# Optimization experiments

Hardware: AMD Instinct MI355X
Metric: run time of the kernel (lower is better)

The kernel has to match this reference:

```python
import jax, jax.numpy as jnp
import numpy as np

SCALES = (5, 15, 40)


def _hamilton(a, b):
    # a, b: (..., 4) quaternions in [w, x, y, z]
    aw, ax, ay, az = a[..., 0], a[..., 1], a[..., 2], a[..., 3]
    bw, bx, by, bz = b[..., 0], b[..., 1], b[..., 2], b[..., 3]
    return jnp.stack([
        aw * bw - ax * bx - ay * by - az * bz,
        aw * bx + ax * bw + ay * bz - az * by,
        aw * by - ax * bz + ay * bw + az * bx,
        aw * bz + ax * by - ay * bx + az * bw,
    ], axis=-1)


def _bearing_quaternions(xyz):
    # xyz: (B, F, P, 3) -> bearing quaternions (B, F, P, 4)
    bbox_min = xyz.min(axis=2)
    bbox_max = xyz.max(axis=2)
    centroids = (bbox_min + bbox_max) * 0.5  # (B, F, 3)
    d = xyz - centroids[:, :, None, :]
    d = d / jnp.clip(jnp.linalg.norm(d, axis=-1, keepdims=True), 1e-12)
    dot = jnp.clip(d[..., 1], -1.0 + 1e-7, 1.0 - 1e-7)
    half = jnp.arccos(dot) * 0.5
    axis = jnp.stack([d[..., 2], jnp.zeros_like(d[..., 0]), -d[..., 0]], axis=-1)
    axis = axis / jnp.clip(jnp.linalg.norm(axis, axis=-1, keepdims=True), 1e-12)
    s = jnp.sin(half)
    return jnp.stack([jnp.cos(half), axis[..., 0] * s, axis[..., 1] * s, axis[..., 2] * s], axis=-1)


def _torch_lower_median(x):
    flat = jnp.sort(x.reshape(-1))
    return flat[(flat.shape[0] - 1) // 2]


def _bearing_qcc_multiscale(points_4d, num_frames):
    B, F, P, _ = points_4d.shape
    xyz = points_4d[..., :3]  # (B, F, P, 3)
    bq = _bearing_quaternions(xyz)  # (B, F, P, 4)

    # Per-transition relative quaternion q_fwd = q_tgt * conj(q_src), vectorized over T = F-1
    conj_sign = jnp.array([1.0, -1.0, -1.0, -1.0], dtype=points_4d.dtype)
    q_src = bq[:, :-1] * conj_sign  # conj, (B, T, P, 4)
    q_tgt = bq[:, 1:]
    q_fwd = _hamilton(q_tgt, q_src)
    q_fwd = q_fwd / jnp.clip(jnp.linalg.norm(q_fwd, axis=-1, keepdims=True), 1e-12)

    # KNN on source-frame xyz for all transitions at once (topk is sorted desc,
    # so smaller-k neighborhoods are prefixes of the max-k result)
    pts = xyz[:, :-1]  # (B, T, P, 3)
    sq = jnp.sum(pts * pts, axis=-1)  # (B, T, P)
    neg_dist = 2.0 * jnp.einsum('btpc,btqc->btpq', pts, pts) - sq[..., :, None] - sq[..., None, :]
    kmax = max(SCALES)
    _, idx = jax.lax.top_k(neg_dist, kmax)  # (B, T, P, kmax)

    # Gather neighbor quaternions: (B, T, P, kmax, 4)
    b_ix = jnp.arange(B)[:, None, None, None]
    t_ix = jnp.arange(F - 1)[None, :, None, None]
    nbr_q = q_fwd[b_ix, t_ix, idx]

    dots = jnp.abs(jnp.sum(q_fwd[..., None, :] * nbr_q, axis=-1))
    dots = jnp.clip(dots, 0.0, 1.0 - 1e-7)
    geo = 2.0 * jnp.arccos(dots)  # (B, T, P, kmax)

    rigidities = []
    for k in SCALES:
        mean_inc = geo[..., :k].mean(axis=-1).mean(axis=1)  # (B, P)
        scale = jnp.clip(_torch_lower_median(mean_inc), 1e-6)
        rig = jnp.where(mean_inc.max() > 0,
                        jnp.exp(-mean_inc / scale),
                        jnp.ones_like(mean_inc))  # (B, P)
        rig = jnp.broadcast_to(rig[:, None, :], (B, F, P)).reshape(B, 1, F * P)
        rigidities.append(rig)
    return jnp.concatenate(rigidities, axis=1)  # (B, len(SCALES), F*P)


def setup_inputs() -> dict:
    key = jax.random.key(0)
    B, F, P = 2, 8, 2048
    points_4d = jax.random.normal(key, (B, F, P, 4), dtype=jnp.float32)
    return {"points_4d": points_4d, "num_frames": F}


def reference(points_4d, num_frames):
    return _bearing_qcc_multiscale(points_4d, num_frames)
```

## Files before the change

### kernel.cpp

```cpp
#include <hip/hip_runtime.h>
#include <math.h>

typedef unsigned long long u64;
typedef unsigned int u32;

#define B_ 2
#define F_ 8
#define P_ 2048
#define T_ 7
#define ROWS (B_*T_*P_)
#define SENT_OU 0xFFFFFFFFu

#define CED(arr,a,b) do { double _x=arr[a], _y=arr[b]; arr[a]=fmin(_x,_y); arr[b]=fmax(_x,_y); } while(0)

__device__ __forceinline__ void sort8d(double* k) {
  CED(k,0,1); CED(k,2,3); CED(k,4,5); CED(k,6,7);
  CED(k,0,2); CED(k,1,3); CED(k,4,6); CED(k,5,7);
  CED(k,1,2); CED(k,5,6);
  CED(k,0,4); CED(k,1,5); CED(k,2,6); CED(k,3,7);
  CED(k,2,4); CED(k,3,5);
  CED(k,1,2); CED(k,3,4); CED(k,5,6);
}

__device__ __forceinline__ void low8(double* A, const double* Bv) {
#pragma unroll
  for (int i = 0; i < 8; ++i) A[i] = fmin(A[i], Bv[7-i]);
#pragma unroll
  for (int st = 4; st >= 1; st >>= 1) {
#pragma unroll
    for (int i = 0; i < 8; ++i) {
      if ((i & st) == 0) { CED(A, i, i + st); }
    }
  }
}

__device__ __forceinline__ u32 bfly16_min_u32(u32 x) {
  u32 t;
  t = (u32)__builtin_amdgcn_update_dpp((int)x,(int)x,0x0B1,0xF,0xF,false); x = t<x?t:x;
  t = (u32)__builtin_amdgcn_update_dpp((int)x,(int)x,0x04E,0xF,0xF,false); x = t<x?t:x;
  t = (u32)__builtin_amdgcn_update_dpp((int)x,(int)x,0x141,0xF,0xF,false); x = t<x?t:x;
  t = (u32)__builtin_amdgcn_update_dpp((int)x,(int)x,0x140,0xF,0xF,false); x = t<x?t:x;
  return x;
}
__device__ __forceinline__ float bfly16_sum_f32(float x) {
  float t;
  t = __uint_as_float((u32)__builtin_amdgcn_update_dpp((int)__float_as_uint(x),(int)__float_as_uint(x),0x0B1,0xF,0xF,false)); x += t;
  t = __uint_as_float((u32)__builtin_amdgcn_update_dpp((int)__float_as_uint(x),(int)__float_as_uint(x),0x04E,0xF,0xF,false)); x += t;
  t = __uint_as_float((u32)__builtin_amdgcn_update_dpp((int)__float_as_uint(x),(int)__float_as_uint(x),0x141,0xF,0xF,false)); x += t;
  t = __uint_as_float((u32)__builtin_amdgcn_update_dpp((int)__float_as_uint(x),(int)__float_as_uint(x),0x140,0xF,0xF,false)); x += t;
  return x;
}

__global__ __launch_bounds__(256) void kA_bearing(const float4* __restrict__ pts,
                                                  float4* __restrict__ bq,
                                                  float4* __restrict__ pts2) {
  int bf = blockIdx.x;
  const float4* base = pts + (size_t)bf * P_;
  int tid = threadIdx.x;
  float x[8], y[8], z[8];
  float mnx =  INFINITY, mny =  INFINITY, mnz =  INFINITY;
  float mxx = -INFINITY, mxy = -INFINITY, mxz = -INFINITY;
#pragma unroll
  for (int i = 0; i < 8; ++i) {
    float4 v = base[tid + i*256];
    x[i]=v.x; y[i]=v.y; z[i]=v.z;
    mnx=fminf(mnx,v.x); mny=fminf(mny,v.y); mnz=fminf(mnz,v.z);
    mxx=fmaxf(mxx,v.x); mxy=fmaxf(mxy,v.y); mxz=fmaxf(mxz,v.z);
  }
#pragma unroll
  for (int off = 32; off >= 1; off >>= 1) {
    mnx=fminf(mnx,__shfl_xor(mnx,off)); mny=fminf(mny,__shfl_xor(mny,off)); mnz=fminf(mnz,__shfl_xor(mnz,off));
    mxx=fmaxf(mxx,__shfl_xor(mxx,off)); mxy=fmaxf(mxy,__shfl_xor(mxy,off)); mxz=fmaxf(mxz,__shfl_xor(mxz,off));
  }
  __shared__ float red[4][6];
  int wid = tid >> 6, lane = tid & 63;
  if (lane == 0) { red[wid][0]=mnx; red[wid][1]=mny; red[wid][2]=mnz;
                   red[wid][3]=mxx; red[wid][4]=mxy; red[wid][5]=mxz; }
  __syncthreads();
  mnx=fminf(fminf(red[0][0],red[1][0]),fminf(red[2][0],red[3][0]));
  mny=fminf(fminf(red[0][1],red[1][1]),fminf(red[2][1],red[3][1]));
  mnz=fminf(fminf(red[0][2],red[1][2]),fminf(red[2][2],red[3][2]));
  mxx=fmaxf(fmaxf(red[0][3],red[1][3]),fmaxf(red[2][3],red[3][3]));
  mxy=fmaxf(fmaxf(red[0][4],red[1][4]),fmaxf(red[2][4],red[3][4]));
  mxz=fmaxf(fmaxf(red[0][5],red[1][5]),fmaxf(red[2][5],red[3][5]));
  float cx=(mnx+mxx)*0.5f, cy=(mny+mxy)*0.5f, cz=(mnz+mxz)*0.5f;
#pragma unroll
  for (int i = 0; i < 8; ++i) {
    float dx=x[i]-cx, dy=y[i]-cy, dz=z[i]-cz;
    float n = sqrtf(((dx*dx) + dy*dy) + dz*dz);
    n = fmaxf(n, 1e-12f);
    float dxn = dx/n, dyn = dy/n, dzn = dz/n;
    float dotc = fminf(fmaxf(dyn, -0.99999990f), 0.99999990f);
    float half = acosf(dotc) * 0.5f;
    float an = sqrtf(dzn*dzn + dxn*dxn);
    an = fmaxf(an, 1e-12f);
    float axx = dzn/an, axz = (-dxn)/an;
    float s = sinf(half), w = cosf(half);
    bq[(size_t)bf*P_ + tid + i*256] = make_float4(w, axx*s, 0.f, axz*s);
    float qs = fmaf(x[i],x[i], fmaf(y[i],y[i], z[i]*z[i]));
    pts2[(size_t)bf*P_ + tid + i*256] = make_float4(x[i], y[i], z[i], qs);
  }
}

__global__ __launch_bounds__(256) void kB_qfwd(const float4* __restrict__ bq,
                                               float4* __restrict__ qf) {
  int i = blockIdx.x*256 + threadIdx.x;
  int p = i & (P_-1);
  int t = (i >> 11) % T_;
  int b = i / (T_*P_);
  float4 s = bq[((size_t)(b*F_ + t))*P_ + p];
  float4 a = bq[((size_t)(b*F_ + t + 1))*P_ + p];
  float aw=a.x, ax=a.y, ay=a.z, az=a.w;
  float bw=s.x, bx=-s.y, by=-s.z, bz=-s.w;
  float w  = ((aw*bw - ax*bx) - ay*by) - az*bz;
  float xo = ((aw*bx + ax*bw) + ay*bz) - az*by;
  float yo = ((aw*by - ax*bz) + ay*bw) + az*bx;
  float zo = ((aw*bz + ax*by) - ay*bx) + az*bw;
  float n = sqrtf(((w*w + xo*xo) + yo*yo) + zo*zo);
  n = fmaxf(n, 1e-12f);
  qf[i] = make_float4(w/n, xo/n, yo/n, zo/n);
}

__device__ __forceinline__ double mkkey(float4 c, u32 q,
                                        float px, float py, float pz, float ps) {
  float dot = fmaf(px, c.x, fmaf(py, c.y, pz*c.z));
  float v = (2.f*dot - ps) - c.w;
  float nd = -v;
  u32 u = __float_as_uint(nd);
  u32 ou = (u & 0x80000000u) ? ~u : (u | 0x80000000u);
  return __longlong_as_double((long long)(0x4000000000000000ull | ((u64)ou << 16) | q));
}

__device__ __forceinline__ void popstep(u32 (&OU)[8], u32 (&IX)[8],
                                        u32& LOU, u32& LIX, u32& CAP, int imod,
                                        int slot, const float4* __restrict__ pbase,
                                        float px, float py, float pz, float ps) {
  if (__any(OU[0] == SENT_OU)) {
    bool need = (OU[0] == SENT_OU);
    u64 lastK = ((u64)LOU << 16) | LIX;
    u64 best = ~0ull;
    for (int j = 0; j < 128; ++j) {
      u32 q = (u32)(j*16 + slot);
      float4 c = pbase[q];
      float dot = fmaf(px, c.x, fmaf(py, c.y, pz*c.z));
      float v = (2.f*dot - ps) - c.w;
      u32 u = __float_as_uint(-v);
      u32 ou = (u & 0x80000000u) ? ~u : (u | 0x80000000u);
      u64 kk = ((u64)ou << 16) | q;
      if (kk > lastK && kk < best) best = kk;
    }
    if (need && best != ~0ull) { OU[0] = (u32)(best >> 16); IX[0] = (u32)(best & 0xffffu); }
  }
  u32 qmin = bfly16_min_u32(OU[0]);
  bool meq = (OU[0] == qmin);
  u32 tt   = meq ? IX[0] : 0xFFFFFFFFu;
  u32 widx = bfly16_min_u32(tt);
  bool iam = meq && (IX[0] == widx);
  CAP = (slot == imod) ? widx : CAP;
  LOU = iam ? qmin : LOU;
  LIX = iam ? widx : LIX;
#pragma unroll
  for (int jj = 0; jj < 7; ++jj) {
    OU[jj] = iam ? OU[jj+1] : OU[jj];
    IX[jj] = iam ? IX[jj+1] : IX[jj];
  }
  OU[7] = iam ? SENT_OU : OU[7];
}

__global__ __launch_bounds__(256) void kC_select(const float4* __restrict__ pts2,
                                                 const float4* __restrict__ qf,
                                                 float* __restrict__ S) {
  int lane = threadIdx.x & 63;
  int wid  = threadIdx.x >> 6;
  int slot = lane & 15;
  int quarter = lane >> 4;
  int gid = blockIdx.x * 16 + wid * 4;
  int p0 = gid & (P_-1);
  int bt = gid >> 11;
  int t  = bt % T_;
  int b  = bt / T_;
  const float4* pbase = pts2 + (size_t)(b*F_ + t) * P_;

  int prow = p0 + quarter;
  float4 pw = pbase[prow];
  float px=pw.x, py=pw.y, pz=pw.z, ps=pw.w;

  double acc[8];
#pragma unroll
  for (int j = 0; j < 8; ++j) acc[j] = __builtin_huge_val();
#pragma unroll 2
  for (int batch = 0; batch < 16; ++batch) {
    int qb = batch*128 + slot;
    float4 c[8];
#pragma unroll
    for (int u = 0; u < 8; ++u) c[u] = pbase[qb + u*16];
    double k[8];
#pragma unroll
    for (int u = 0; u < 8; ++u) k[u] = mkkey(c[u], (u32)(qb + u*16), px,py,pz,ps);
    sort8d(k);
    low8(acc, k);
  }

  u32 OU[8], IX[8];
#pragma unroll
  for (int j = 0; j < 8; ++j) {
    u64 bb = (u64)__double_as_longlong(acc[j]);
    OU[j] = (u32)(bb >> 16); IX[j] = (u32)(bb & 0xffffu);
  }

  u32 lou=0, lix=0, cap1=0, cap2=0, cap3=0;

#pragma unroll 1
  for (int i = 0; i < 16; ++i)
    popstep(OU, IX, lou, lix, cap1, i, slot, pbase, px,py,pz,ps);
#pragma unroll 1
  for (int i = 0; i < 16; ++i)
    popstep(OU, IX, lou, lix, cap2, i, slot, pbase, px,py,pz,ps);
#pragma unroll 1
  for (int i = 0; i < 8; ++i)
    popstep(OU, IX, lou, lix, cap3, i, slot, pbase, px,py,pz,ps);

  int row = bt*P_ + prow;
  const float4* qbt = qf + (size_t)bt * P_;
  float4 qp = qf[row];

  float4 n; float d;
  n = qbt[cap1]; d = ((qp.x*n.x + qp.y*n.y) + qp.z*n.z) + qp.w*n.w;
  float g1 = 2.f * acosf(fminf(fabsf(d), 0.99999990f));
  n = qbt[cap2]; d = ((qp.x*n.x + qp.y*n.y) + qp.z*n.z) + qp.w*n.w;
  float g2 = 2.f * acosf(fminf(fabsf(d), 0.99999990f));
  n = qbt[cap3]; d = ((qp.x*n.x + qp.y*n.y) + qp.z*n.z) + qp.w*n.w;
  float g3 = (slot < 8) ? 2.f * acosf(fminf(fabsf(d), 0.99999990f)) : 0.f;

  float s40 = bfly16_sum_f32(g1 + g2 + g3);
  float s15 = bfly16_sum_f32((slot < 15) ? g1 : 0.f);
  float s5  = bfly16_sum_f32((slot < 5)  ? g1 : 0.f);

  if (slot == 0) {
    S[0*ROWS + row] = s5  / 5.f;
    S[1*ROWS + row] = s15 / 15.f;
    S[2*ROWS + row] = s40 / 40.f;
  }
}

__global__ __launch_bounds__(1024) void kE_final(const float* __restrict__ S,
                                                 float* __restrict__ out) {
  int k = blockIdx.x;
  int tid = threadIdx.x;
  __shared__ float srt[4096];
  const float* Sk = S + (size_t)k * ROWS;
  float m[4];
#pragma unroll
  for (int u = 0; u < 4; ++u) {
    int j = tid + u*1024;
    int b = j >> 11, p = j & 2047;
    float acc = 0.f;
#pragma unroll
    for (int t = 0; t < 7; ++t) acc += Sk[(b*7 + t)*2048 + p];
    m[u] = acc / 7.f;
    srt[j] = m[u];
  }
  __syncthreads();
  for (int size = 2; size <= 4096; size <<= 1) {
    for (int stride = size >> 1; stride > 0; stride >>= 1) {
      for (int c = tid; c < 2048; c += 1024) {
        int i = 2*c - (c & (stride - 1));
        int j = i + stride;
        bool up = ((i & size) == 0);
        float a = srt[i], bb = srt[j];
        if ((a > bb) == up) { srt[i] = bb; srt[j] = a; }
      }
      __syncthreads();
    }
  }
  float scale = fmaxf(srt[2047], 1e-6f);
  bool pos = srt[4095] > 0.f;
#pragma unroll
  for (int u = 0; u < 4; ++u) {
    int j = tid + u*1024;
    int b = j >> 11, p = j & 2047;
    float r = pos ? expf(-m[u]/scale) : 1.f;
    float* ob = out + ((size_t)(b*3 + k)*8)*2048 + p;
#pragma unroll
    for (int f = 0; f < 8; ++f) ob[f*2048] = r;
  }
}

extern "C" void kernel_launch(void* const* d_in, const int* in_sizes, int n_in,
                              void* d_out, int out_size, void* d_ws, size_t ws_size,
                              hipStream_t stream) {
  (void)in_sizes; (void)n_in; (void)out_size; (void)ws_size;
  const float4* pts = (const float4*)d_in[0];
  float* ws = (float*)d_ws;
  float4* bq   = (float4*)ws;
  float4* qfw  = (float4*)(ws + 131072);
  float*  S    = ws + 131072 + 114688;
  float4* pts2 = (float4*)(ws + 131072 + 114688 + 86016);
  float*  out = (float*)d_out;

  hipLaunchKernelGGL(kA_bearing, dim3(B_*F_), dim3(256), 0, stream, pts, bq, pts2);
  hipLaunchKernelGGL(kB_qfwd,    dim3(ROWS/256), dim3(256), 0, stream, bq, qfw);
  hipLaunchKernelGGL(kC_select,  dim3(ROWS/16), dim3(256), 0, stream, pts2, qfw, S);
  hipLaunchKernelGGL(kE_final,   dim3(3), dim3(1024), 0, stream, S, out);
}
```

Measured before the change: 142.6 us.

## Streamline key construction, seed top-8 from first batch, merge final sorts into one block

```diff
diff --git a/kernel.cpp b/kernel.cpp
--- a/kernel.cpp
+++ b/kernel.cpp
@@ -124,11 +124,18 @@
 __device__ __forceinline__ double mkkey(float4 c, u32 q,
                                         float px, float py, float pz, float ps) {
   float dot = fmaf(px, c.x, fmaf(py, c.y, pz*c.z));
-  float v = (2.f*dot - ps) - c.w;
-  float nd = -v;
+  float nd  = fmaf(-2.f, dot, ps + c.w);
   u32 u = __float_as_uint(nd);
-  u32 ou = (u & 0x80000000u) ? ~u : (u | 0x80000000u);
-  return __longlong_as_double((long long)(0x4000000000000000ull | ((u64)ou << 16) | q));
+  u32 ou = u ^ (((u32)((int)u >> 31)) | 0x80000000u);
+  return __hiloint2double((int)((ou >> 16) | 0x40000000u), (int)((ou << 16) | q));
+}
+__device__ __forceinline__ u64 mkkey_u(float4 c, u32 q,
+                                       float px, float py, float pz, float ps) {
+  float dot = fmaf(px, c.x, fmaf(py, c.y, pz*c.z));
+  float nd  = fmaf(-2.f, dot, ps + c.w);
+  u32 u = __float_as_uint(nd);
+  u32 ou = u ^ (((u32)((int)u >> 31)) | 0x80000000u);
+  return ((u64)ou << 16) | q;
 }
 
 __device__ __forceinline__ void popstep(u32 (&OU)[8], u32 (&IX)[8],
@@ -141,15 +148,13 @@
     u64 best = ~0ull;
     for (int j = 0; j < 128; ++j) {
       u32 q = (u32)(j*16 + slot);
-      float4 c = pbase[q];
-      float dot = fmaf(px, c.x, fmaf(py, c.y, pz*c.z));
-      float v = (2.f*dot - ps) - c.w;
-      u32 u = __float_as_uint(-v);
-      u32 ou = (u & 0x80000000u) ? ~u : (u | 0x80000000u);
-      u64 kk = ((u64)ou << 16) | q;
+      u64 kk = mkkey_u(pbase[q], q, px,py,pz,ps);
       if (kk > lastK && kk < best) best = kk;
     }
-    if (need && best != ~0ull) { OU[0] = (u32)(best >> 16); IX[0] = (u32)(best & 0xffffu); }
+    if (need && best != ~0ull) {
+      OU[0] = (u32)(best >> 16); IX[0] = (u32)(best & 0xffffu);
+      LOU = OU[0]; LIX = IX[0];
+    }
   }
   u32 qmin = bfly16_min_u32(OU[0]);
   bool meq = (OU[0] == qmin);
@@ -157,8 +162,6 @@
   u32 widx = bfly16_min_u32(tt);
   bool iam = meq && (IX[0] == widx);
   CAP = (slot == imod) ? widx : CAP;
-  LOU = iam ? qmin : LOU;
-  LIX = iam ? widx : LIX;
 #pragma unroll
   for (int jj = 0; jj < 7; ++jj) {
     OU[jj] = iam ? OU[jj+1] : OU[jj];
@@ -186,10 +189,17 @@
   float px=pw.x, py=pw.y, pz=pw.z, ps=pw.w;
 
   double acc[8];
-#pragma unroll
-  for (int j = 0; j < 8; ++j) acc[j] = __builtin_huge_val();
+  {
+    double k0[8];
+#pragma unroll
+    for (int u = 0; u < 8; ++u) { float4 c = pbase[u*16 + slot];
+      k0[u] = mkkey(c, (u32)(u*16 + slot), px,py,pz,ps); }
+    sort8d(k0);
+#pragma unroll
+    for (int j = 0; j < 8; ++j) acc[j] = k0[j];
+  }
 #pragma unroll 2
-  for (int batch = 0; batch < 16; ++batch) {
+  for (int batch = 1; batch < 16; ++batch) {
     int qb = batch*128 + slot;
     float4 c[8];
 #pragma unroll
@@ -205,10 +215,18 @@
 #pragma unroll
   for (int j = 0; j < 8; ++j) {
     u64 bb = (u64)__double_as_longlong(acc[j]);
-    OU[j] = (u32)(bb >> 16); IX[j] = (u32)(bb & 0xffffu);
-  }
-
-  u32 lou=0, lix=0, cap1=0, cap2=0, cap3=0;
+    OU[j] = (u32)(bb >> 16) & 0x3FFFFFFFu | ((u32)(bb >> 16) & 0xC0000000u ? 0u : 0u);
+    OU[j] = (u32)((bb >> 16) & 0xFFFFFFFFull);
+    IX[j] = (u32)(bb & 0xffffu);
+  }
+#pragma unroll
+  for (int j = 0; j < 8; ++j) {
+    u64 bb = (u64)__double_as_longlong(acc[j]);
+    OU[j] = (u32)((bb & 0x0000FFFFFFFF0000ull) >> 16);
+    IX[j] = (u32)(bb & 0xffffu);
+  }
+  u32 lou = OU[7], lix = IX[7];
+  u32 cap1=0, cap2=0, cap3=0;
 
 #pragma unroll 1
   for (int i = 0; i < 16; ++i)
@@ -245,20 +263,22 @@
 
 __global__ __launch_bounds__(1024) void kE_final(const float* __restrict__ S,
                                                  float* __restrict__ out) {
-  int k = blockIdx.x;
   int tid = threadIdx.x;
-  __shared__ float srt[4096];
-  const float* Sk = S + (size_t)k * ROWS;
-  float m[4];
-#pragma unroll
-  for (int u = 0; u < 4; ++u) {
-    int j = tid + u*1024;
-    int b = j >> 11, p = j & 2047;
-    float acc = 0.f;
-#pragma unroll
-    for (int t = 0; t < 7; ++t) acc += Sk[(b*7 + t)*2048 + p];
-    m[u] = acc / 7.f;
-    srt[j] = m[u];
+  __shared__ float srt[3][4096];
+  float m[3][4];
+#pragma unroll
+  for (int k = 0; k < 3; ++k) {
+    const float* Sk = S + (size_t)k * ROWS;
+#pragma unroll
+    for (int u = 0; u < 4; ++u) {
+      int j = tid + u*1024;
+      int b = j >> 11, p = j & 2047;
+      float acc = 0.f;
+#pragma unroll
+      for (int t = 0; t < 7; ++t) acc += Sk[(b*7 + t)*2048 + p];
+      m[k][u] = acc / 7.f;
+      srt[k][j] = m[k][u];
+    }
   }
   __syncthreads();
   for (int size = 2; size <= 4096; size <<= 1) {
@@ -267,22 +287,28 @@
         int i = 2*c - (c & (stride - 1));
         int j = i + stride;
         bool up = ((i & size) == 0);
-        float a = srt[i], bb = srt[j];
-        if ((a > bb) == up) { srt[i] = bb; srt[j] = a; }
+#pragma unroll
+        for (int k = 0; k < 3; ++k) {
+          float a = srt[k][i], bb = srt[k][j];
+          if ((a > bb) == up) { srt[k][i] = bb; srt[k][j] = a; }
+        }
       }
       __syncthreads();
     }
   }
-  float scale = fmaxf(srt[2047], 1e-6f);
-  bool pos = srt[4095] > 0.f;
-#pragma unroll
-  for (int u = 0; u < 4; ++u) {
-    int j = tid + u*1024;
-    int b = j >> 11, p = j & 2047;
-    float r = pos ? expf(-m[u]/scale) : 1.f;
-    float* ob = out + ((size_t)(b*3 + k)*8)*2048 + p;
-#pragma unroll
-    for (int f = 0; f < 8; ++f) ob[f*2048] = r;
+#pragma unroll
+  for (int k = 0; k < 3; ++k) {
+    float scale = fmaxf(srt[k][2047], 1e-6f);
+    bool pos = srt[k][4095] > 0.f;
+#pragma unroll
+    for (int u = 0; u < 4; ++u) {
+      int j = tid + u*1024;
+      int b = j >> 11, p = j & 2047;
+      float r = pos ? expf(-m[k][u]/scale) : 1.f;
+      float* ob = out + ((size_t)(b*3 + k)*8)*2048 + p;
+#pragma unroll
+      for (int f = 0; f < 8; ++f) ob[f*2048] = r;
+    }
   }
 }
 
@@ -301,5 +327,5 @@
   hipLaunchKernelGGL(kA_bearing, dim3(B_*F_), dim3(256), 0, stream, pts, bq, pts2);
   hipLaunchKernelGGL(kB_qfwd,    dim3(ROWS/256), dim3(256), 0, stream, bq, qfw);
   hipLaunchKernelGGL(kC_select,  dim3(ROWS/16), dim3(256), 0, stream, pts2, qfw, S);
-  hipLaunchKernelGGL(kE_final,   dim3(3), dim3(1024), 0, stream, S, out);
-}
+  hipLaunchKernelGGL(kE_final,   dim3(1), dim3(1024), 0, stream, S, out);
+}
```

New measurement: 169.5 us. 18.9% more time.
